# Kernel optimization log

Measured on AMD Instinct MI355X. Metric: run time of the kernel, lower is better.

The kernel has to match this reference:

```python
import jax, jax.numpy as jnp
import numpy as np

PAD_IDX, EOS_IDX, SOS_IDX = 0, 1, 2
NEG = -10000.0


def setup_inputs() -> dict:
    key = jax.random.key(0)
    k1, k2, k3 = jax.random.split(key, 3)
    B, T, K = 64, 2048, 256
    y = jax.random.normal(k1, (B, T, K), dtype=jnp.float32)
    # transition matrix initialized as in crf.__init__
    trans = jax.random.normal(k2, (K, K), dtype=jnp.float32)
    trans = trans.at[SOS_IDX, :].set(NEG)
    trans = trans.at[:, EOS_IDX].set(NEG)
    trans = trans.at[:, PAD_IDX].set(NEG)
    trans = trans.at[PAD_IDX, :].set(NEG)
    trans = trans.at[PAD_IDX, EOS_IDX].set(0.0)
    trans = trans.at[PAD_IDX, PAD_IDX].set(0.0)
    # variable-length float mask (1.0 for valid steps), as the module expects
    lengths = jax.random.randint(k3, (B,), T // 2, T + 1)
    mask = (jnp.arange(T)[None, :] < lengths[:, None]).astype(jnp.float32)
    return {"y": y, "mask": mask, "trans": trans}


def reference(y, mask, trans):
    # Linear-chain CRF partition function (forward algorithm in log space).
    # new_score[b,i] = y[b,t,i] + logsumexp_j(score[b,j] + trans[i,j])
    B, T, K = y.shape
    score0 = jnp.full((B, K), NEG, dtype=y.dtype).at[:, SOS_IDX].set(0.0)

    def step(score, xs):
        emit_t, mask_t = xs  # [B,K], [B]
        # score[b,None,j] + trans[None,i,j] -> lse over j
        new = emit_t + jax.scipy.special.logsumexp(
            score[:, None, :] + trans[None, :, :], axis=-1)
        m = mask_t[:, None]
        score = new * m + score * (1.0 - m)
        return score, None

    score, _ = jax.lax.scan(step, score0,
                            (jnp.swapaxes(y, 0, 1), mask.T))  # scan over T
    return jax.scipy.special.logsumexp(score, axis=-1)  # [B]
```

## Files before the change

### kernel.cpp

```cpp
#include <hip/hip_runtime.h>
#include <hip/hip_bf16.h>


typedef _Float16 h2 __attribute__((ext_vector_type(2)));
typedef _Float16 h8 __attribute__((ext_vector_type(8)));

#define TT 2048
#define KK 256
#define NTHREADS 256
#define SOS_IDX 2
#define CH 8

#define FDOT2(a, b, c) __builtin_amdgcn_fdot2((a), (b), (c), false)

__global__ __launch_bounds__(NTHREADS, 1)
void crf_fwd_kernel(const float* __restrict__ y, const float* __restrict__ mask,
                    const float* __restrict__ trans, float* __restrict__ out) {
    const int b = blockIdx.x;
    const int k = threadIdx.x;
    const int lane = k & 63;
    const int wave = k >> 6;

    __shared__ __align__(16) _Float16 Pb[2][KK];
    __shared__ float sred[4];

    h2 e[KK / 2];
    {
        const float4* tr = (const float4*)(trans + (size_t)k * KK);
        #pragma unroll
        for (int i = 0; i < KK / 4; ++i) {
            float4 v = tr[i];
            h2 a, c;
            a[0] = (_Float16)__expf(v.x);
            a[1] = (_Float16)__expf(v.y);
            c[0] = (_Float16)__expf(v.z);
            c[1] = (_Float16)__expf(v.w);
            e[2 * i]     = a;
            e[2 * i + 1] = c;
        }
    }

    float lsum = 0.f;
    {
        const float* mrow = mask + (size_t)b * TT;
        #pragma unroll
        for (int i = 0; i < TT / NTHREADS; ++i) lsum += mrow[k + i * NTHREADS];
        #pragma unroll
        for (int off = 32; off >= 1; off >>= 1) lsum += __shfl_xor(lsum, off, 64);
        if (lane == 0) sred[wave] = lsum;
    }

    Pb[0][k] = (_Float16)((k == SOS_IDX) ? 1.f : 0.f);
    __syncthreads();
    const int L = (int)(sred[0] + sred[1] + sred[2] + sred[3] + 0.5f);

    const float* yrow = y + (size_t)b * TT * KK + k;
    float Lam = 0.f;
    int cur = 0;
    const h2 ones = {(_Float16)1.f, (_Float16)1.f};

    for (int t0 = 0; t0 < L; t0 += CH) {
        float yv[CH];
        #pragma unroll
        for (int u = 0; u < CH; ++u) yv[u] = yrow[(size_t)(t0 + u) * KK];
        const int nst = (L - t0 < CH) ? (L - t0) : CH;

        #pragma unroll
        for (int u = 0; u < CH; ++u) {
            if (u < nst) {
                float ey = __expf(yv[u]);

                float q0 = 0.f, q1 = 0.f, q2 = 0.f, q3 = 0.f;
                float s0 = 0.f, s1 = 0.f, s2 = 0.f, s3 = 0.f;
                const h8* Pv = (const h8*)Pb[cur];
                #pragma unroll
                for (int c = 0; c < KK / 8; ++c) {
                    h8 pv = Pv[c];
                    h2 p0 = {pv[0], pv[1]}, p1 = {pv[2], pv[3]};
                    h2 p2 = {pv[4], pv[5]}, p3 = {pv[6], pv[7]};
                    q0 = FDOT2(e[4 * c + 0], p0, q0);
                    q1 = FDOT2(e[4 * c + 1], p1, q1);
                    q2 = FDOT2(e[4 * c + 2], p2, q2);
                    q3 = FDOT2(e[4 * c + 3], p3, q3);
                    s0 = FDOT2(ones, p0, s0);
                    s1 = FDOT2(ones, p1, s1);
                    s2 = FDOT2(ones, p2, s2);
                    s3 = FDOT2(ones, p3, s3);
                }
                float q = (q0 + q1) + (q2 + q3);
                float S = (s0 + s1) + (s2 + s3);

                float f = __builtin_amdgcn_rcpf(S) * 0.03125f;
                float pn = ey * q * f;
                Pb[cur ^ 1][k] = (_Float16)pn;
                Lam += __log2f(S);
                cur ^= 1;
                __syncthreads();
            }
        }
    }

    {
        float s0 = 0.f, s1 = 0.f, s2 = 0.f, s3 = 0.f;
        const h8* Pv = (const h8*)Pb[cur];
        #pragma unroll
        for (int c = 0; c < KK / 8; ++c) {
            h8 pv = Pv[c];
            h2 p0 = {pv[0], pv[1]}, p1 = {pv[2], pv[3]};
            h2 p2 = {pv[4], pv[5]}, p3 = {pv[6], pv[7]};
            s0 = FDOT2(ones, p0, s0);
            s1 = FDOT2(ones, p1, s1);
            s2 = FDOT2(ones, p2, s2);
            s3 = FDOT2(ones, p3, s3);
        }
        float Sf = (s0 + s1) + (s2 + s3);
        if (k == 0) {
            out[b] = 0.69314718056f * (__log2f(Sf) + Lam + 5.0f * (float)L);
        }
    }
}

extern "C" void kernel_launch(void* const* d_in, const int* in_sizes, int n_in,
                              void* d_out, int out_size, void* d_ws, size_t ws_size,
                              hipStream_t stream) {
    const float* y     = (const float*)d_in[0];
    const float* mask  = (const float*)d_in[1];
    const float* trans = (const float*)d_in[2];
    float* out = (float*)d_out;
    const int B = in_sizes[1] / TT;
    crf_fwd_kernel<<<B, NTHREADS, 0, stream>>>(y, mask, trans, out);
}
```

Before: 1.751 ms.

## Compute CRF forward matvec with MFMA across 8 waves and fused row-sum reduction

```diff
diff --git a/kernel.cpp b/kernel.cpp
--- a/kernel.cpp
+++ b/kernel.cpp
@@ -1,122 +1,141 @@
 #include <hip/hip_runtime.h>
-#include <hip/hip_bf16.h>
 
 
-typedef _Float16 h2 __attribute__((ext_vector_type(2)));
-typedef _Float16 h8 __attribute__((ext_vector_type(8)));
+typedef _Float16 f16x8 __attribute__((ext_vector_type(8)));
+typedef _Float16 f16x4 __attribute__((ext_vector_type(4)));
+typedef float    f32x4 __attribute__((ext_vector_type(4)));
 
 #define TT 2048
 #define KK 256
-#define NTHREADS 256
+#define NTH 512
+#define NW (NTH / 64)
 #define SOS_IDX 2
-#define CH 8
+#define CSCALE 0.03125f
 
-#define FDOT2(a, b, c) __builtin_amdgcn_fdot2((a), (b), (c), false)
+__global__ __launch_bounds__(NTH, 2)
+void crf_fwd_kernel(const float* __restrict__ y, const float* __restrict__ mask,
+                    const float* __restrict__ trans, float* __restrict__ out)
+{
+    const int tid = threadIdx.x;
+    const int b   = blockIdx.x;
+    const int w   = tid >> 6;
+    const int l   = tid & 63;
+    const int m16 = l & 15;
+    const int s   = l >> 4;
+    const bool act = (m16 == 0);
 
-__global__ __launch_bounds__(NTHREADS, 1)
-void crf_fwd_kernel(const float* __restrict__ y, const float* __restrict__ mask,
-                    const float* __restrict__ trans, float* __restrict__ out) {
-    const int b = blockIdx.x;
-    const int k = threadIdx.x;
-    const int lane = k & 63;
-    const int wave = k >> 6;
+    __shared__ __align__(16) _Float16 Wbuf[2][KK];
+    __shared__ __align__(16) float    sred[2][16];
+    __shared__ float sl[NW];
 
-    __shared__ __align__(16) _Float16 Pb[2][KK];
-    __shared__ float sred[4];
-
-    h2 e[KK / 2];
-    {
-        const float4* tr = (const float4*)(trans + (size_t)k * KK);
+    f16x8 af[2][8];
+    #pragma unroll
+    for (int rt = 0; rt < 2; ++rt) {
+        const float* tr = trans + (size_t)(32 * w + 16 * rt + m16) * KK + 8 * s;
         #pragma unroll
-        for (int i = 0; i < KK / 4; ++i) {
-            float4 v = tr[i];
-            h2 a, c;
-            a[0] = (_Float16)__expf(v.x);
-            a[1] = (_Float16)__expf(v.y);
-            c[0] = (_Float16)__expf(v.z);
-            c[1] = (_Float16)__expf(v.w);
-            e[2 * i]     = a;
-            e[2 * i + 1] = c;
-        }
-    }
-
-    float lsum = 0.f;
-    {
-        const float* mrow = mask + (size_t)b * TT;
-        #pragma unroll
-        for (int i = 0; i < TT / NTHREADS; ++i) lsum += mrow[k + i * NTHREADS];
-        #pragma unroll
-        for (int off = 32; off >= 1; off >>= 1) lsum += __shfl_xor(lsum, off, 64);
-        if (lane == 0) sred[wave] = lsum;
-    }
-
-    Pb[0][k] = (_Float16)((k == SOS_IDX) ? 1.f : 0.f);
-    __syncthreads();
-    const int L = (int)(sred[0] + sred[1] + sred[2] + sred[3] + 0.5f);
-
-    const float* yrow = y + (size_t)b * TT * KK + k;
-    float Lam = 0.f;
-    int cur = 0;
-    const h2 ones = {(_Float16)1.f, (_Float16)1.f};
-
-    for (int t0 = 0; t0 < L; t0 += CH) {
-        float yv[CH];
-        #pragma unroll
-        for (int u = 0; u < CH; ++u) yv[u] = yrow[(size_t)(t0 + u) * KK];
-        const int nst = (L - t0 < CH) ? (L - t0) : CH;
-
-        #pragma unroll
-        for (int u = 0; u < CH; ++u) {
-            if (u < nst) {
-                float ey = __expf(yv[u]);
-
-                float q0 = 0.f, q1 = 0.f, q2 = 0.f, q3 = 0.f;
-                float s0 = 0.f, s1 = 0.f, s2 = 0.f, s3 = 0.f;
-                const h8* Pv = (const h8*)Pb[cur];
-                #pragma unroll
-                for (int c = 0; c < KK / 8; ++c) {
-                    h8 pv = Pv[c];
-                    h2 p0 = {pv[0], pv[1]}, p1 = {pv[2], pv[3]};
-                    h2 p2 = {pv[4], pv[5]}, p3 = {pv[6], pv[7]};
-                    q0 = FDOT2(e[4 * c + 0], p0, q0);
-                    q1 = FDOT2(e[4 * c + 1], p1, q1);
-                    q2 = FDOT2(e[4 * c + 2], p2, q2);
-                    q3 = FDOT2(e[4 * c + 3], p3, q3);
-                    s0 = FDOT2(ones, p0, s0);
-                    s1 = FDOT2(ones, p1, s1);
-                    s2 = FDOT2(ones, p2, s2);
-                    s3 = FDOT2(ones, p3, s3);
-                }
-                float q = (q0 + q1) + (q2 + q3);
-                float S = (s0 + s1) + (s2 + s3);
-
-                float f = __builtin_amdgcn_rcpf(S) * 0.03125f;
-                float pn = ey * q * f;
-                Pb[cur ^ 1][k] = (_Float16)pn;
-                Lam += __log2f(S);
-                cur ^= 1;
-                __syncthreads();
-            }
+        for (int kt = 0; kt < 8; ++kt) {
+            float4 v0 = *(const float4*)(tr + 32 * kt);
+            float4 v1 = *(const float4*)(tr + 32 * kt + 4);
+            f16x8 a;
+            a[0] = (_Float16)__expf(v0.x); a[1] = (_Float16)__expf(v0.y);
+            a[2] = (_Float16)__expf(v0.z); a[3] = (_Float16)__expf(v0.w);
+            a[4] = (_Float16)__expf(v1.x); a[5] = (_Float16)__expf(v1.y);
+            a[6] = (_Float16)__expf(v1.z); a[7] = (_Float16)__expf(v1.w);
+            af[rt][kt] = a;
         }
     }
 
     {
-        float s0 = 0.f, s1 = 0.f, s2 = 0.f, s3 = 0.f;
-        const h8* Pv = (const h8*)Pb[cur];
+        float lsum = 0.f;
+        const float* mrow = mask + (size_t)b * TT;
         #pragma unroll
-        for (int c = 0; c < KK / 8; ++c) {
-            h8 pv = Pv[c];
-            h2 p0 = {pv[0], pv[1]}, p1 = {pv[2], pv[3]};
-            h2 p2 = {pv[4], pv[5]}, p3 = {pv[6], pv[7]};
-            s0 = FDOT2(ones, p0, s0);
-            s1 = FDOT2(ones, p1, s1);
-            s2 = FDOT2(ones, p2, s2);
-            s3 = FDOT2(ones, p3, s3);
+        for (int i = 0; i < TT / NTH; ++i) lsum += mrow[tid + i * NTH];
+        #pragma unroll
+        for (int off = 32; off >= 1; off >>= 1) lsum += __shfl_xor(lsum, off, 64);
+        if (l == 0) sl[w] = lsum;
+    }
+
+    if (tid < KK) Wbuf[0][tid] = (_Float16)((tid == SOS_IDX) ? 1.f : 0.f);
+    if (tid < 16) sred[0][tid] = 0.0625f;
+    __syncthreads();
+
+    float Ls = 0.f;
+    #pragma unroll
+    for (int i = 0; i < NW; ++i) Ls += sl[i];
+    const int L = (int)(Ls + 0.5f);
+
+    const float* yb = y + (size_t)b * TT * KK + 32 * w + 4 * s;
+    float Lam = 0.f;
+
+    f16x8 bf[8];
+    {
+        const f16x8 fz = {(_Float16)0.f, (_Float16)0.f, (_Float16)0.f, (_Float16)0.f,
+                          (_Float16)0.f, (_Float16)0.f, (_Float16)0.f, (_Float16)0.f};
+        #pragma unroll
+        for (int i = 0; i < 8; ++i) bf[i] = fz;
+    }
+
+    float4 yA0, yA1, yB0, yB1;
+    if (act) { yA0 = *(const float4*)yb; yA1 = *(const float4*)(yb + 16); }
+
+    auto STEP = [&](int t, const float4 yc0, const float4 yc1, float4& yn0, float4& yn1) {
+        const int par = t & 1;
+        float g = 0.f;
+        if (act) {
+            const int tn = (t + 1 < L) ? (t + 1) : (L - 1);
+            yn0 = *(const float4*)(yb + (size_t)tn * KK);
+            yn1 = *(const float4*)(yb + (size_t)tn * KK + 16);
+            const f16x8* Wv = (const f16x8*)Wbuf[par];
+            #pragma unroll
+            for (int kt = 0; kt < 8; ++kt) bf[kt] = Wv[4 * kt + s];
+            const float4* sp = (const float4*)sred[par];
+            float4 p0 = sp[0], p1 = sp[1], p2 = sp[2], p3 = sp[3];
+            float Sg = ((p0.x + p0.y) + (p0.z + p0.w)) + ((p1.x + p1.y) + (p1.z + p1.w))
+                     + ((p2.x + p2.y) + (p2.z + p2.w)) + ((p3.x + p3.y) + (p3.z + p3.w));
+            Lam += __log2f(Sg);
+            g = CSCALE * __builtin_amdgcn_rcpf(Sg);
         }
-        float Sf = (s0 + s1) + (s2 + s3);
-        if (k == 0) {
-            out[b] = 0.69314718056f * (__log2f(Sf) + Lam + 5.0f * (float)L);
+        f32x4 c0a = {0.f, 0.f, 0.f, 0.f}, c0b = c0a, c1a = c0a, c1b = c0a;
+        #pragma unroll
+        for (int kt = 0; kt < 4; ++kt) {
+            c0a = __builtin_amdgcn_mfma_f32_16x16x32_f16(af[0][kt],     bf[kt],     c0a, 0, 0, 0);
+            c1a = __builtin_amdgcn_mfma_f32_16x16x32_f16(af[1][kt],     bf[kt],     c1a, 0, 0, 0);
+            c0b = __builtin_amdgcn_mfma_f32_16x16x32_f16(af[0][kt + 4], bf[kt + 4], c0b, 0, 0, 0);
+            c1b = __builtin_amdgcn_mfma_f32_16x16x32_f16(af[1][kt + 4], bf[kt + 4], c1b, 0, 0, 0);
         }
+        if (act) {
+            const f32x4 c0 = c0a + c0b, c1 = c1a + c1b;
+            float w0 = __expf(yc0.x) * c0[0] * g;
+            float w1 = __expf(yc0.y) * c0[1] * g;
+            float w2 = __expf(yc0.z) * c0[2] * g;
+            float w3 = __expf(yc0.w) * c0[3] * g;
+            float w4 = __expf(yc1.x) * c1[0] * g;
+            float w5 = __expf(yc1.y) * c1[1] * g;
+            float w6 = __expf(yc1.z) * c1[2] * g;
+            float w7 = __expf(yc1.w) * c1[3] * g;
+            f16x4 h0 = {(_Float16)w0, (_Float16)w1, (_Float16)w2, (_Float16)w3};
+            f16x4 h1 = {(_Float16)w4, (_Float16)w5, (_Float16)w6, (_Float16)w7};
+            *(f16x4*)&Wbuf[par ^ 1][32 * w + 4 * s]      = h0;
+            *(f16x4*)&Wbuf[par ^ 1][32 * w + 16 + 4 * s] = h1;
+            float ps = ((w0 + w1) + (w2 + w3)) + ((w4 + w5) + (w6 + w7));
+            ps += __shfl_xor(ps, 16, 64);
+            if ((l & 31) == 0) sred[par ^ 1][2 * w + (l >> 5)] = ps;
+        }
+        asm volatile("s_waitcnt lgkmcnt(0)" ::: "memory");
+        __builtin_amdgcn_s_barrier();
+    };
+
+    for (int t = 0; t < L; t += 2) {
+        STEP(t, yA0, yA1, yB0, yB1);
+        if (t + 1 < L) STEP(t + 1, yB0, yB1, yA0, yA1);
+    }
+
+    if (tid == 0) {
+        const float* sp = sred[L & 1];
+        float Sf = 0.f;
+        #pragma unroll
+        for (int i = 0; i < 16; ++i) Sf += sp[i];
+        out[b] = 0.69314718056f * (Lam + __log2f(Sf) + 5.0f * (float)L);
     }
 }
 
@@ -128,5 +147,5 @@
     const float* trans = (const float*)d_in[2];
     float* out = (float*)d_out;
     const int B = in_sizes[1] / TT;
-    crf_fwd_kernel<<<B, NTHREADS, 0, stream>>>(y, mask, trans, out);
+    crf_fwd_kernel<<<B, NTH, 0, stream>>>(y, mask, trans, out);
 }
```

After: 1.921 ms. 1.1x slower.
